# Kernel tuning notes

Measured on AMD Instinct MI355X. Metric: run time of the kernel, lower is better.

## Reference

```python
import jax, jax.numpy as jnp
import numpy as np

N_LAYERS = 2
D_MODEL = 1024
D_INNER = 2 * D_MODEL
D_STATE = 16
D_CONV = 4
DT_RANK = D_MODEL // 16  # 64
B_SZ, L = 1, 2048
EPS = 1e-5


def layernorm(x, w, b):
    mu = jnp.mean(x, axis=-1, keepdims=True)
    var = jnp.mean(jnp.square(x - mu), axis=-1, keepdims=True)
    return (x - mu) * jax.lax.rsqrt(var + EPS) * w + b


def mamba(x, in_w, cw, cb, xp_w, dtp_w, dtp_b, A_log, Dp, out_w):
    # x: [B, L, D_MODEL]
    Bn, Ln, _ = x.shape
    xz = jnp.einsum('bld,ed->ble', x, in_w)          # [B,L,2*D_INNER]
    xc, z = jnp.split(xz, 2, axis=-1)
    # causal depthwise conv1d (kernel D_CONV)
    xp = jnp.pad(xc, ((0, 0), (D_CONV - 1, 0), (0, 0)))
    xc = sum(xp[:, k:k + Ln, :] * cw[:, k] for k in range(D_CONV)) + cb
    xc = jax.nn.silu(xc)
    dbl = jnp.einsum('ble,re->blr', xc, xp_w)        # [B,L,DT_RANK+2*D_STATE]
    dt, Bm, Cm = jnp.split(dbl, [DT_RANK, DT_RANK + D_STATE], axis=-1)
    dt = jax.nn.softplus(jnp.einsum('blr,er->ble', dt, dtp_w) + dtp_b)  # [B,L,E]
    A = -jnp.exp(A_log)                              # [E,N], strictly negative
    dA = jnp.exp(dt[..., None] * A)                  # [B,L,E,N]
    dBu = (dt * xc)[..., None] * Bm[:, :, None, :]   # [B,L,E,N]

    def step(h, inp):
        dA_t, dBu_t, C_t = inp
        h = dA_t * h + dBu_t                         # [B,E,N]
        y = jnp.einsum('ben,bn->be', h, C_t)
        return h, y

    h0 = jnp.zeros((Bn, D_INNER, D_STATE), dA.dtype)
    _, ys = jax.lax.scan(step, h0, (dA.transpose(1, 0, 2, 3),
                                    dBu.transpose(1, 0, 2, 3),
                                    Cm.transpose(1, 0, 2)))
    y = ys.transpose(1, 0, 2) + xc * Dp              # [B,L,E]
    y = y * jax.nn.silu(z)
    return jnp.einsum('ble,de->bld', y, out_w)       # [B,L,D_MODEL]


def setup_inputs() -> dict:
    key = jax.random.key(0)
    ks = jax.random.split(key, 12)
    s = 0.02
    dt_init = np.log(np.expm1(0.01)).astype(np.float32)  # softplus^-1(0.01)
    A_row = jnp.log(jnp.arange(1, D_STATE + 1, dtype=jnp.float32))
    return {
        'x': jax.random.normal(ks[0], (B_SZ, L, D_MODEL), jnp.float32),
        'ln_w': jnp.ones((N_LAYERS, D_MODEL), jnp.float32),
        'ln_b': jnp.zeros((N_LAYERS, D_MODEL), jnp.float32),
        'in_proj_w': jax.random.normal(ks[1], (N_LAYERS, 2 * D_INNER, D_MODEL)) * s,
        'conv_w': jax.random.normal(ks[2], (N_LAYERS, D_INNER, D_CONV)) * 0.2,
        'conv_b': jnp.zeros((N_LAYERS, D_INNER), jnp.float32),
        'x_proj_w': jax.random.normal(ks[3], (N_LAYERS, DT_RANK + 2 * D_STATE, D_INNER)) * s,
        'dt_proj_w': jax.random.normal(ks[4], (N_LAYERS, D_INNER, DT_RANK)) * (DT_RANK ** -0.5),
        'dt_proj_b': jnp.full((N_LAYERS, D_INNER), dt_init),
        'A_log': jnp.broadcast_to(A_row, (N_LAYERS, D_INNER, D_STATE)).copy(),
        'D_skip': jnp.ones((N_LAYERS, D_INNER), jnp.float32),
        'out_proj_w': jax.random.normal(ks[5], (N_LAYERS, D_MODEL, D_INNER)) * s,
        'norm_f_w': jnp.ones((D_MODEL,), jnp.float32),
        'norm_f_b': jnp.zeros((D_MODEL,), jnp.float32),
    }


def reference(x, ln_w, ln_b, in_proj_w, conv_w, conv_b, x_proj_w, dt_proj_w,
              dt_proj_b, A_log, D_skip, out_proj_w, norm_f_w, norm_f_b):
    for i in range(N_LAYERS):
        h = layernorm(x, ln_w[i], ln_b[i])
        h = mamba(h, in_proj_w[i], conv_w[i], conv_b[i], x_proj_w[i],
                  dt_proj_w[i], dt_proj_b[i], A_log[i], D_skip[i], out_proj_w[i])
        x = h + x  # residual (dropout/drop_path are identity in eval)
    return layernorm(x, norm_f_w, norm_f_b)
```

## Files before the change

### kernel.cpp

```cpp
#include <hip/hip_runtime.h>
#include <hip/hip_bf16.h>
#include <math.h>

#define LSEQ 2048
#define DMODEL 1024
#define DINNER 2048
#define DSTATE 16
#define DCONV 4
#define DTRANK 64
#define RPROJ 96

#define CHUNK 32
#define NCHUNK (LSEQ / CHUNK)

#define XSPLIT 4

typedef __attribute__((ext_vector_type(8))) short bf16x8;
typedef __attribute__((ext_vector_type(4))) float f32x4;

__device__ __forceinline__ float softplusf(float x) {
    return (x > 20.f) ? x : log1pf(__expf(x));
}
__device__ __forceinline__ float siluf(float x) {
    return x / (1.f + __expf(-x));
}
__device__ __forceinline__ short f2bf(float f) {
    union { float f; unsigned u; } v; v.f = f;
    unsigned r = v.u + 0x7FFFu + ((v.u >> 16) & 1u);
    return (short)(r >> 16);
}
__device__ __forceinline__ float bf2f(short h) {
    union { unsigned u; float f; } v;
    v.u = ((unsigned)(unsigned short)h) << 16;
    return v.f;
}

__device__ __forceinline__ void cvt8(const float* __restrict__ s,
                                     short* __restrict__ d, int i) {
    const float4 a = *(const float4*)(s + i);
    const float4 b = *(const float4*)(s + i + 4);
    alignas(16) short h[8];
    h[0] = f2bf(a.x); h[1] = f2bf(a.y); h[2] = f2bf(a.z); h[3] = f2bf(a.w);
    h[4] = f2bf(b.x); h[5] = f2bf(b.y); h[6] = f2bf(b.z); h[7] = f2bf(b.w);
    *(uint4*)(d + i) = *(const uint4*)h;
}

__global__ __launch_bounds__(256) void cvt_weights(
    const float* __restrict__ s0, short* __restrict__ d0, int n0,
    const float* __restrict__ s1, short* __restrict__ d1, int n1,
    const float* __restrict__ s2, short* __restrict__ d2, int n2,
    const float* __restrict__ s3, short* __restrict__ d3, int n3)
{
    int i = (blockIdx.x * 256 + threadIdx.x) * 8;
    if (i < n0) { cvt8(s0, d0, i); return; }
    i -= n0;
    if (i < n1) { cvt8(s1, d1, i); return; }
    i -= n1;
    if (i < n2) { cvt8(s2, d2, i); return; }
    i -= n2;
    if (i < n3) { cvt8(s3, d3, i); return; }
}

__global__ __launch_bounds__(256) void ln_kernel(
    const float* __restrict__ x, const float* __restrict__ w,
    const float* __restrict__ b, float* __restrict__ outf,
    short* __restrict__ outb)
{
    __shared__ float s1[256], s2[256];
    const int row = blockIdx.x;
    const int tid = threadIdx.x;
    const float* xr = x + (size_t)row * DMODEL;
    float v[4];
    float s = 0.f, sq = 0.f;
#pragma unroll
    for (int k = 0; k < 4; k++) {
        v[k] = xr[k * 256 + tid];
        s += v[k];
        sq += v[k] * v[k];
    }
    s1[tid] = s; s2[tid] = sq;
    __syncthreads();
    for (int off = 128; off > 0; off >>= 1) {
        if (tid < off) { s1[tid] += s1[tid + off]; s2[tid] += s2[tid + off]; }
        __syncthreads();
    }
    const float mu = s1[0] * (1.f / DMODEL);
    const float var = s2[0] * (1.f / DMODEL) - mu * mu;
    const float rstd = rsqrtf(var + 1e-5f);
#pragma unroll
    for (int k = 0; k < 4; k++) {
        const int i = k * 256 + tid;
        const float o = (v[k] - mu) * rstd * w[i] + b[i];
        if (outf) outf[(size_t)row * DMODEL + i] = o;
        if (outb) outb[(size_t)row * DMODEL + i] = f2bf(o);
    }
}

template<int MODE>
__global__ __launch_bounds__(256) void gemm_mfma(
    const short* __restrict__ A, int lda,
    const short* __restrict__ W, int ldw,
    float* __restrict__ Cf, short* __restrict__ Cb, int ldc,
    int M, int N, int K,
    const float* __restrict__ bias,
    const float* __restrict__ resid,
    size_t csplit)
{
    __shared__ alignas(16) short As[64 * 32];
    __shared__ alignas(16) short Ws[64 * 32];

    const int tid = threadIdx.x;
    const int lane = tid & 63;
    const int w = tid >> 6;
    const int wr = w >> 1, wc = w & 1;
    const int row0 = blockIdx.y * 64;
    const int col0 = blockIdx.x * 64;
    const int kbeg = blockIdx.z * K;

    const int srow = tid >> 2;
    const int skch = ((tid & 3) ^ ((srow >> 1) & 3)) * 8;

    f32x4 acc[2][2];
#pragma unroll
    for (int i = 0; i < 2; i++)
#pragma unroll
        for (int j = 0; j < 2; j++) acc[i][j] = (f32x4)0.f;

    const int lrow = lane & 15;
    const int q = lane >> 4;
    const int wrow = col0 + srow;

    for (int kt = kbeg; kt < kbeg + K; kt += 32) {
        __syncthreads();
        {
            const short* gp = A + (size_t)(row0 + srow) * lda + kt + skch;
            __builtin_amdgcn_global_load_lds(
                (const __attribute__((address_space(1))) void*)gp,
                (__attribute__((address_space(3))) void*)(As + tid * 8), 16, 0, 0);
        }
        if (wrow < N) {
            const short* gp = W + (size_t)wrow * ldw + kt + skch;
            __builtin_amdgcn_global_load_lds(
                (const __attribute__((address_space(1))) void*)gp,
                (__attribute__((address_space(3))) void*)(Ws + tid * 8), 16, 0, 0);
        }
        __syncthreads();

        bf16x8 af[2], bfr[2];
#pragma unroll
        for (int i = 0; i < 2; i++) {
            const int R = wr * 32 + i * 16 + lrow;
            af[i] = *(const bf16x8*)&As[R * 32 + ((q ^ ((R >> 1) & 3)) * 8)];
        }
#pragma unroll
        for (int j = 0; j < 2; j++) {
            const int R = wc * 32 + j * 16 + lrow;
            bfr[j] = *(const bf16x8*)&Ws[R * 32 + ((q ^ ((R >> 1) & 3)) * 8)];
        }
#pragma unroll
        for (int i = 0; i < 2; i++)
#pragma unroll
            for (int j = 0; j < 2; j++)
                acc[i][j] = __builtin_amdgcn_mfma_f32_16x16x32_bf16(
                    af[i], bfr[j], acc[i][j], 0, 0, 0);
    }

    if (MODE == 0 && csplit) Cf += blockIdx.z * csplit;

    const int rbase = row0 + wr * 32;
    const int cbase = col0 + wc * 32;
#pragma unroll
    for (int i = 0; i < 2; i++) {
#pragma unroll
        for (int j = 0; j < 2; j++) {
            const int gcol = cbase + j * 16 + lrow;
            if (gcol < N) {
#pragma unroll
                for (int r = 0; r < 4; r++) {
                    const int grow = rbase + i * 16 + (lane >> 4) * 4 + r;
                    float v = acc[i][j][r];
                    if (MODE == 1) v = softplusf(v + bias[gcol]);
                    if (MODE == 2) v += resid[(size_t)grow * ldc + gcol];
                    if (MODE == 3) {
                        Cb[(size_t)grow * ldc + gcol] = f2bf(v);
                    } else {
                        Cf[(size_t)grow * ldc + gcol] = v;
                    }
                }
            }
        }
    }
}

__global__ __launch_bounds__(256) void combine_xproj(
    const float* __restrict__ part,
    float* __restrict__ dbl, short* __restrict__ dblb)
{
    const int i = (blockIdx.x * 256 + threadIdx.x) * 4;
    const int S = LSEQ * RPROJ;
    float4 v = *(const float4*)(part + i);
#pragma unroll
    for (int s = 1; s < XSPLIT; s++) {
        const float4 p = *(const float4*)(part + s * S + i);
        v.x += p.x; v.y += p.y; v.z += p.z; v.w += p.w;
    }
    *(float4*)(dbl + i) = v;
    alignas(8) short h[4] = {f2bf(v.x), f2bf(v.y), f2bf(v.z), f2bf(v.w)};
    *(unsigned long long*)(dblb + i) = *(const unsigned long long*)h;
}

__global__ __launch_bounds__(256) void conv_silu_kernel(
    const short* __restrict__ xzb, const float* __restrict__ cw,
    const float* __restrict__ cb, short* __restrict__ xcb)
{
    const int g = blockIdx.x * 256 + threadIdx.x;
    const int t = g >> 8;
    const int c0 = (g & 255) * 8;
    float acc[8];
#pragma unroll
    for (int j = 0; j < 8; j++) acc[j] = cb[c0 + j];
#pragma unroll
    for (int k = 0; k < DCONV; k++) {
        const int tt = t - (DCONV - 1) + k;
        if (tt >= 0) {
            const bf16x8 v = *(const bf16x8*)(xzb + (size_t)tt * (2 * DINNER) + c0);
#pragma unroll
            for (int j = 0; j < 8; j++)
                acc[j] += bf2f(v[j]) * cw[(c0 + j) * DCONV + k];
        }
    }
    alignas(16) short h[8];
#pragma unroll
    for (int j = 0; j < 8; j++) h[j] = f2bf(siluf(acc[j]));
    *(uint4*)(xcb + (size_t)t * DINNER + c0) = *(const uint4*)h;
}

__global__ __launch_bounds__(256) void scan_pass1(
    const float* __restrict__ dt,
    const short* __restrict__ xcb,
    const float* __restrict__ dbl,
    const float* __restrict__ A_log,
    float* __restrict__ S,
    float* __restrict__ sumdt)
{
    const int e = blockIdx.x * 256 + threadIdx.x;
    const int c = blockIdx.y;
    float a[DSTATE];
#pragma unroll
    for (int n = 0; n < DSTATE; n++) a[n] = -__expf(A_log[(size_t)e * DSTATE + n]);
    float h[DSTATE];
#pragma unroll
    for (int n = 0; n < DSTATE; n++) h[n] = 0.f;
    float sd = 0.f;

    __shared__ float sBC[CHUNK][32];
    for (int i = threadIdx.x; i < CHUNK * 32; i += 256) {
        const int tl = i >> 5, j = i & 31;
        sBC[tl][j] = dbl[(size_t)(c * CHUNK + tl) * RPROJ + DTRANK + j];
    }
    __syncthreads();

    for (int tl = 0; tl < CHUNK; tl++) {
        const int t = c * CHUNK + tl;
        const float dtv = dt[(size_t)t * DINNER + e];
        const float du = dtv * bf2f(xcb[(size_t)t * DINNER + e]);
        sd += dtv;
#pragma unroll
        for (int n = 0; n < DSTATE; n++) {
            const float dA = __expf(dtv * a[n]);
            h[n] = dA * h[n] + du * sBC[tl][n];
        }
    }
    sumdt[(size_t)c * DINNER + e] = sd;
#pragma unroll
    for (int n = 0; n < DSTATE; n++)
        S[((size_t)c * DSTATE + n) * DINNER + e] = h[n];
}

__global__ __launch_bounds__(256) void scan_pass2(
    const float* __restrict__ A_log,
    const float* __restrict__ sumdt,
    float* __restrict__ S)
{
    const int idx = blockIdx.x * 256 + threadIdx.x;
    const int e = idx & (DINNER - 1);
    const int n = idx >> 11;
    const float a = -__expf(A_log[(size_t)e * DSTATE + n]);
    float H = 0.f;
    for (int c = 0; c < NCHUNK; c++) {
        const size_t off = ((size_t)c * DSTATE + n) * DINNER + e;
        const float tmp = S[off];
        S[off] = H;
        const float P = __expf(a * sumdt[(size_t)c * DINNER + e]);
        H = P * H + tmp;
    }
}

__global__ __launch_bounds__(256) void scan_pass3(
    const float* __restrict__ dt,
    const short* __restrict__ xcb,
    const float* __restrict__ dbl,
    const short* __restrict__ xzb,
    const float* __restrict__ A_log,
    const float* __restrict__ Dp,
    const float* __restrict__ S,
    short* __restrict__ yb)
{
    const int e = blockIdx.x * 256 + threadIdx.x;
    const int c = blockIdx.y;
    float a[DSTATE];
#pragma unroll
    for (int n = 0; n < DSTATE; n++) a[n] = -__expf(A_log[(size_t)e * DSTATE + n]);
    float h[DSTATE];
#pragma unroll
    for (int n = 0; n < DSTATE; n++)
        h[n] = S[((size_t)c * DSTATE + n) * DINNER + e];
    const float dskip = Dp[e];

    __shared__ float sBC[CHUNK][32];
    for (int i = threadIdx.x; i < CHUNK * 32; i += 256) {
        const int tl = i >> 5, j = i & 31;
        sBC[tl][j] = dbl[(size_t)(c * CHUNK + tl) * RPROJ + DTRANK + j];
    }
    __syncthreads();

    for (int tl = 0; tl < CHUNK; tl++) {
        const int t = c * CHUNK + tl;
        const float dtv = dt[(size_t)t * DINNER + e];
        const float xcv = bf2f(xcb[(size_t)t * DINNER + e]);
        const float du = dtv * xcv;
        float yv = 0.f;
#pragma unroll
        for (int n = 0; n < DSTATE; n++) {
            const float dA = __expf(dtv * a[n]);
            h[n] = dA * h[n] + du * sBC[tl][n];
            yv += h[n] * sBC[tl][16 + n];
        }
        const float zv = bf2f(xzb[(size_t)t * (2 * DINNER) + DINNER + e]);
        yv = (yv + xcv * dskip) * siluf(zv);
        yb[(size_t)t * DINNER + e] = f2bf(yv);
    }
}

extern "C" void kernel_launch(void* const* d_in, const int* in_sizes, int n_in,
                              void* d_out, int out_size, void* d_ws, size_t ws_size,
                              hipStream_t stream) {
    const float* x_in   = (const float*)d_in[0];
    const float* ln_w   = (const float*)d_in[1];
    const float* ln_b   = (const float*)d_in[2];
    const float* in_w   = (const float*)d_in[3];
    const float* conv_w = (const float*)d_in[4];
    const float* conv_b = (const float*)d_in[5];
    const float* xp_w   = (const float*)d_in[6];
    const float* dtp_w  = (const float*)d_in[7];
    const float* dtp_b  = (const float*)d_in[8];
    const float* A_log  = (const float*)d_in[9];
    const float* D_skip = (const float*)d_in[10];
    const float* out_w  = (const float*)d_in[11];
    const float* nf_w   = (const float*)d_in[12];
    const float* nf_b   = (const float*)d_in[13];
    float* out = (float*)d_out;

    float* w = (float*)d_ws;
    float* buf_x = w; w += (size_t)LSEQ * DMODEL;
    float* dbl   = w; w += (size_t)LSEQ * RPROJ;
    float* xpart = w; w += (size_t)XSPLIT * LSEQ * RPROJ;
    float* dtb   = w; w += (size_t)LSEQ * DINNER;
    float* Sbuf  = w; w += (size_t)NCHUNK * DSTATE * DINNER;
    float* sumdt = w; w += (size_t)NCHUNK * DINNER;
    short* h_bf    = (short*)w; w += (size_t)LSEQ * DMODEL / 2;
    short* xz_bf   = (short*)w; w += (size_t)LSEQ * 2 * DINNER / 2;
    short* xc_bf   = (short*)w; w += (size_t)LSEQ * DINNER / 2;
    short* y_bf    = (short*)w; w += (size_t)LSEQ * DINNER / 2;
    short* dbl_bf  = (short*)w; w += (size_t)LSEQ * RPROJ / 2 + 1;
    short* in_w_bf  = (short*)w; w += (size_t)2 * (2 * DINNER) * DMODEL / 2;
    short* xp_w_bf  = (short*)w; w += (size_t)2 * RPROJ * DINNER / 2;
    short* dtp_w_bf = (short*)w; w += (size_t)2 * DINNER * DTRANK / 2;
    short* out_w_bf = (short*)w; w += (size_t)2 * DMODEL * DINNER / 2;

    {
        const int n1 = 2 * (2 * DINNER) * DMODEL;
        const int n2 = 2 * RPROJ * DINNER;
        const int n3 = 2 * DMODEL * DINNER;
        const int n4 = 2 * DINNER * DTRANK;
        const int total = n1 + n2 + n3 + n4;
        cvt_weights<<<dim3(total / (256 * 8)), dim3(256), 0, stream>>>(
            in_w, in_w_bf, n1, xp_w, xp_w_bf, n2,
            out_w, out_w_bf, n3, dtp_w, dtp_w_bf, n4);
    }

    for (int layer = 0; layer < 2; layer++) {
        const float* resid_src = (layer == 0) ? x_in : buf_x;
        ln_kernel<<<dim3(LSEQ), dim3(256), 0, stream>>>(
            resid_src, ln_w + layer * DMODEL, ln_b + layer * DMODEL,
            nullptr, h_bf);
        gemm_mfma<3><<<dim3((2 * DINNER) / 64, LSEQ / 64), dim3(256), 0, stream>>>(
            h_bf, DMODEL, in_w_bf + (size_t)layer * 2 * DINNER * DMODEL, DMODEL,
            nullptr, xz_bf, 2 * DINNER, LSEQ, 2 * DINNER, DMODEL, nullptr, nullptr, 0);
        conv_silu_kernel<<<dim3((LSEQ * DINNER / 8) / 256), dim3(256), 0, stream>>>(
            xz_bf, conv_w + (size_t)layer * DINNER * DCONV, conv_b + layer * DINNER,
            xc_bf);
        gemm_mfma<0><<<dim3(2, LSEQ / 64, XSPLIT), dim3(256), 0, stream>>>(
            xc_bf, DINNER, xp_w_bf + (size_t)layer * RPROJ * DINNER, DINNER,
            xpart, nullptr, RPROJ, LSEQ, RPROJ, DINNER / XSPLIT, nullptr, nullptr,
            (size_t)LSEQ * RPROJ);
        combine_xproj<<<dim3((LSEQ * RPROJ / 4) / 256), dim3(256), 0, stream>>>(
            xpart, dbl, dbl_bf);
        gemm_mfma<1><<<dim3(DINNER / 64, LSEQ / 64), dim3(256), 0, stream>>>(
            dbl_bf, RPROJ, dtp_w_bf + (size_t)layer * DINNER * DTRANK, DTRANK,
            dtb, nullptr, DINNER, LSEQ, DINNER, DTRANK,
            dtp_b + layer * DINNER, nullptr, 0);
        const float* Al = A_log + (size_t)layer * DINNER * DSTATE;
        scan_pass1<<<dim3(DINNER / 256, NCHUNK), dim3(256), 0, stream>>>(
            dtb, xc_bf, dbl, Al, Sbuf, sumdt);
        scan_pass2<<<dim3((DINNER * DSTATE) / 256), dim3(256), 0, stream>>>(
            Al, sumdt, Sbuf);
        scan_pass3<<<dim3(DINNER / 256, NCHUNK), dim3(256), 0, stream>>>(
            dtb, xc_bf, dbl, xz_bf, Al, D_skip + layer * DINNER, Sbuf, y_bf);
        gemm_mfma<2><<<dim3(DMODEL / 64, LSEQ / 64), dim3(256), 0, stream>>>(
            y_bf, DINNER, out_w_bf + (size_t)layer * DMODEL * DINNER, DINNER,
            buf_x, nullptr, DMODEL, LSEQ, DMODEL, DINNER, nullptr, resid_src, 0);
    }
    ln_kernel<<<dim3(LSEQ), dim3(256), 0, stream>>>(buf_x, nf_w, nf_b, out, nullptr);
}
```

Baseline: 517.1 us.

## Widen GEMM N-tiles, store dt in bf16, halve scan chunk, prefetch scan inputs

The GEMM kernel is templated on the number of 16-wide column fragments so the in_proj and dt_proj GEMMs use 64x128 tiles. This gives more MFMA work per A-tile load and launches fewer blocks. The dt projection now writes softplus output as bf16 rather than fp32, which halves dt traffic in both scan passes. The scan chunk drops from 32 to 16 to double parallelism, and the per-step loads in the scan passes are software-prefetched one step ahead. The trade-offs are bf16 rounding of dt before the exp, which may hurt accuracy, and twice the chunk-carry work in pass2.

New measurement: 491.1 us. 5.0% less time.

```diff
diff --git a/kernel.cpp b/kernel.cpp
--- a/kernel.cpp
+++ b/kernel.cpp
@@ -10,7 +10,7 @@
 #define DTRANK 64
 #define RPROJ 96
 
-#define CHUNK 32
+#define CHUNK 16
 #define NCHUNK (LSEQ / CHUNK)
 
 #define XSPLIT 4
@@ -96,7 +96,7 @@
     }
 }
 
-template<int MODE>
+template<int NJ, int MODE>
 __global__ __launch_bounds__(256) void gemm_mfma(
     const short* __restrict__ A, int lda,
     const short* __restrict__ W, int ldw,
@@ -106,29 +106,31 @@
     const float* __restrict__ resid,
     size_t csplit)
 {
+    constexpr int BN = 32 * NJ;
+    constexpr int HN = 16 * NJ;
+    constexpr int WISS = BN / 64;
     __shared__ alignas(16) short As[64 * 32];
-    __shared__ alignas(16) short Ws[64 * 32];
+    __shared__ alignas(16) short Ws[BN * 32];
 
     const int tid = threadIdx.x;
     const int lane = tid & 63;
     const int w = tid >> 6;
     const int wr = w >> 1, wc = w & 1;
     const int row0 = blockIdx.y * 64;
-    const int col0 = blockIdx.x * 64;
+    const int col0 = blockIdx.x * BN;
     const int kbeg = blockIdx.z * K;
 
     const int srow = tid >> 2;
     const int skch = ((tid & 3) ^ ((srow >> 1) & 3)) * 8;
 
-    f32x4 acc[2][2];
+    f32x4 acc[2][NJ];
 #pragma unroll
     for (int i = 0; i < 2; i++)
 #pragma unroll
-        for (int j = 0; j < 2; j++) acc[i][j] = (f32x4)0.f;
+        for (int j = 0; j < NJ; j++) acc[i][j] = (f32x4)0.f;
 
     const int lrow = lane & 15;
     const int q = lane >> 4;
-    const int wrow = col0 + srow;
 
     for (int kt = kbeg; kt < kbeg + K; kt += 32) {
         __syncthreads();
@@ -138,29 +140,34 @@
                 (const __attribute__((address_space(1))) void*)gp,
                 (__attribute__((address_space(3))) void*)(As + tid * 8), 16, 0, 0);
         }
-        if (wrow < N) {
-            const short* gp = W + (size_t)wrow * ldw + kt + skch;
-            __builtin_amdgcn_global_load_lds(
-                (const __attribute__((address_space(1))) void*)gp,
-                (__attribute__((address_space(3))) void*)(Ws + tid * 8), 16, 0, 0);
+#pragma unroll
+        for (int j = 0; j < WISS; j++) {
+            const int wrow = col0 + j * 64 + srow;
+            if (wrow < N) {
+                const short* gp = W + (size_t)wrow * ldw + kt + skch;
+                __builtin_amdgcn_global_load_lds(
+                    (const __attribute__((address_space(1))) void*)gp,
+                    (__attribute__((address_space(3))) void*)(Ws + j * 2048 + tid * 8),
+                    16, 0, 0);
+            }
         }
         __syncthreads();
 
-        bf16x8 af[2], bfr[2];
+        bf16x8 af[2], bfr[NJ];
 #pragma unroll
         for (int i = 0; i < 2; i++) {
             const int R = wr * 32 + i * 16 + lrow;
             af[i] = *(const bf16x8*)&As[R * 32 + ((q ^ ((R >> 1) & 3)) * 8)];
         }
 #pragma unroll
-        for (int j = 0; j < 2; j++) {
-            const int R = wc * 32 + j * 16 + lrow;
+        for (int j = 0; j < NJ; j++) {
+            const int R = wc * HN + j * 16 + lrow;
             bfr[j] = *(const bf16x8*)&Ws[R * 32 + ((q ^ ((R >> 1) & 3)) * 8)];
         }
 #pragma unroll
         for (int i = 0; i < 2; i++)
 #pragma unroll
-            for (int j = 0; j < 2; j++)
+            for (int j = 0; j < NJ; j++)
                 acc[i][j] = __builtin_amdgcn_mfma_f32_16x16x32_bf16(
                     af[i], bfr[j], acc[i][j], 0, 0, 0);
     }
@@ -168,20 +175,20 @@
     if (MODE == 0 && csplit) Cf += blockIdx.z * csplit;
 
     const int rbase = row0 + wr * 32;
-    const int cbase = col0 + wc * 32;
+    const int cbase = col0 + wc * HN;
 #pragma unroll
     for (int i = 0; i < 2; i++) {
 #pragma unroll
-        for (int j = 0; j < 2; j++) {
+        for (int j = 0; j < NJ; j++) {
             const int gcol = cbase + j * 16 + lrow;
             if (gcol < N) {
 #pragma unroll
                 for (int r = 0; r < 4; r++) {
                     const int grow = rbase + i * 16 + (lane >> 4) * 4 + r;
                     float v = acc[i][j][r];
-                    if (MODE == 1) v = softplusf(v + bias[gcol]);
                     if (MODE == 2) v += resid[(size_t)grow * ldc + gcol];
-                    if (MODE == 3) {
+                    if (MODE == 5) v = softplusf(v + bias[gcol]);
+                    if (MODE == 3 || MODE == 5) {
                         Cb[(size_t)grow * ldc + gcol] = f2bf(v);
                     } else {
                         Cf[(size_t)grow * ldc + gcol] = v;
@@ -236,7 +243,7 @@
 }
 
 __global__ __launch_bounds__(256) void scan_pass1(
-    const float* __restrict__ dt,
+    const short* __restrict__ dtb,
     const short* __restrict__ xcb,
     const float* __restrict__ dbl,
     const float* __restrict__ A_log,
@@ -260,16 +267,24 @@
     }
     __syncthreads();
 
+    const size_t rb = (size_t)c * CHUNK * DINNER + e;
+    short dt_c = dtb[rb], xc_c = xcb[rb];
+#pragma unroll
     for (int tl = 0; tl < CHUNK; tl++) {
-        const int t = c * CHUNK + tl;
-        const float dtv = dt[(size_t)t * DINNER + e];
-        const float du = dtv * bf2f(xcb[(size_t)t * DINNER + e]);
+        short dt_n = 0, xc_n = 0;
+        if (tl + 1 < CHUNK) {
+            dt_n = dtb[rb + (size_t)(tl + 1) * DINNER];
+            xc_n = xcb[rb + (size_t)(tl + 1) * DINNER];
+        }
+        const float dtv = bf2f(dt_c);
+        const float du = dtv * bf2f(xc_c);
         sd += dtv;
 #pragma unroll
         for (int n = 0; n < DSTATE; n++) {
             const float dA = __expf(dtv * a[n]);
             h[n] = dA * h[n] + du * sBC[tl][n];
         }
+        dt_c = dt_n; xc_c = xc_n;
     }
     sumdt[(size_t)c * DINNER + e] = sd;
 #pragma unroll
@@ -297,7 +312,7 @@
 }
 
 __global__ __launch_bounds__(256) void scan_pass3(
-    const float* __restrict__ dt,
+    const short* __restrict__ dtb,
     const short* __restrict__ xcb,
     const float* __restrict__ dbl,
     const short* __restrict__ xzb,
@@ -324,10 +339,19 @@
     }
     __syncthreads();
 
+    const size_t rb = (size_t)c * CHUNK * DINNER + e;
+    const size_t zb = (size_t)c * CHUNK * (2 * DINNER) + DINNER + e;
+    short dt_c = dtb[rb], xc_c = xcb[rb], z_c = xzb[zb];
+#pragma unroll
     for (int tl = 0; tl < CHUNK; tl++) {
-        const int t = c * CHUNK + tl;
-        const float dtv = dt[(size_t)t * DINNER + e];
-        const float xcv = bf2f(xcb[(size_t)t * DINNER + e]);
+        short dt_n = 0, xc_n = 0, z_n = 0;
+        if (tl + 1 < CHUNK) {
+            dt_n = dtb[rb + (size_t)(tl + 1) * DINNER];
+            xc_n = xcb[rb + (size_t)(tl + 1) * DINNER];
+            z_n = xzb[zb + (size_t)(tl + 1) * (2 * DINNER)];
+        }
+        const float dtv = bf2f(dt_c);
+        const float xcv = bf2f(xc_c);
         const float du = dtv * xcv;
         float yv = 0.f;
 #pragma unroll
@@ -336,9 +360,9 @@
             h[n] = dA * h[n] + du * sBC[tl][n];
             yv += h[n] * sBC[tl][16 + n];
         }
-        const float zv = bf2f(xzb[(size_t)t * (2 * DINNER) + DINNER + e]);
-        yv = (yv + xcv * dskip) * siluf(zv);
-        yb[(size_t)t * DINNER + e] = f2bf(yv);
+        yv = (yv + xcv * dskip) * siluf(bf2f(z_c));
+        yb[rb + (size_t)tl * DINNER] = f2bf(yv);
+        dt_c = dt_n; xc_c = xc_n; z_c = z_n;
     }
 }
 
@@ -365,12 +389,12 @@
     float* buf_x = w; w += (size_t)LSEQ * DMODEL;
     float* dbl   = w; w += (size_t)LSEQ * RPROJ;
     float* xpart = w; w += (size_t)XSPLIT * LSEQ * RPROJ;
-    float* dtb   = w; w += (size_t)LSEQ * DINNER;
     float* Sbuf  = w; w += (size_t)NCHUNK * DSTATE * DINNER;
     float* sumdt = w; w += (size_t)NCHUNK * DINNER;
     short* h_bf    = (short*)w; w += (size_t)LSEQ * DMODEL / 2;
     short* xz_bf   = (short*)w; w += (size_t)LSEQ * 2 * DINNER / 2;
     short* xc_bf   = (short*)w; w += (size_t)LSEQ * DINNER / 2;
+    short* dt_bf   = (short*)w; w += (size_t)LSEQ * DINNER / 2;
     short* y_bf    = (short*)w; w += (size_t)LSEQ * DINNER / 2;
     short* dbl_bf  = (short*)w; w += (size_t)LSEQ * RPROJ / 2 + 1;
     short* in_w_bf  = (short*)w; w += (size_t)2 * (2 * DINNER) * DMODEL / 2;
@@ -394,30 +418,30 @@
         ln_kernel<<<dim3(LSEQ), dim3(256), 0, stream>>>(
             resid_src, ln_w + layer * DMODEL, ln_b + layer * DMODEL,
             nullptr, h_bf);
-        gemm_mfma<3><<<dim3((2 * DINNER) / 64, LSEQ / 64), dim3(256), 0, stream>>>(
+        gemm_mfma<4, 3><<<dim3((2 * DINNER) / 128, LSEQ / 64), dim3(256), 0, stream>>>(
             h_bf, DMODEL, in_w_bf + (size_t)layer * 2 * DINNER * DMODEL, DMODEL,
             nullptr, xz_bf, 2 * DINNER, LSEQ, 2 * DINNER, DMODEL, nullptr, nullptr, 0);
         conv_silu_kernel<<<dim3((LSEQ * DINNER / 8) / 256), dim3(256), 0, stream>>>(
             xz_bf, conv_w + (size_t)layer * DINNER * DCONV, conv_b + layer * DINNER,
             xc_bf);
-        gemm_mfma<0><<<dim3(2, LSEQ / 64, XSPLIT), dim3(256), 0, stream>>>(
+        gemm_mfma<2, 0><<<dim3(2, LSEQ / 64, XSPLIT), dim3(256), 0, stream>>>(
             xc_bf, DINNER, xp_w_bf + (size_t)layer * RPROJ * DINNER, DINNER,
             xpart, nullptr, RPROJ, LSEQ, RPROJ, DINNER / XSPLIT, nullptr, nullptr,
             (size_t)LSEQ * RPROJ);
         combine_xproj<<<dim3((LSEQ * RPROJ / 4) / 256), dim3(256), 0, stream>>>(
             xpart, dbl, dbl_bf);
-        gemm_mfma<1><<<dim3(DINNER / 64, LSEQ / 64), dim3(256), 0, stream>>>(
+        gemm_mfma<4, 5><<<dim3(DINNER / 128, LSEQ / 64), dim3(256), 0, stream>>>(
             dbl_bf, RPROJ, dtp_w_bf + (size_t)layer * DINNER * DTRANK, DTRANK,
-            dtb, nullptr, DINNER, LSEQ, DINNER, DTRANK,
+            nullptr, dt_bf, DINNER, LSEQ, DINNER, DTRANK,
             dtp_b + layer * DINNER, nullptr, 0);
         const float* Al = A_log + (size_t)layer * DINNER * DSTATE;
         scan_pass1<<<dim3(DINNER / 256, NCHUNK), dim3(256), 0, stream>>>(
-            dtb, xc_bf, dbl, Al, Sbuf, sumdt);
+            dt_bf, xc_bf, dbl, Al, Sbuf, sumdt);
         scan_pass2<<<dim3((DINNER * DSTATE) / 256), dim3(256), 0, stream>>>(
             Al, sumdt, Sbuf);
         scan_pass3<<<dim3(DINNER / 256, NCHUNK), dim3(256), 0, stream>>>(
-            dtb, xc_bf, dbl, xz_bf, Al, D_skip + layer * DINNER, Sbuf, y_bf);
-        gemm_mfma<2><<<dim3(DMODEL / 64, LSEQ / 64), dim3(256), 0, stream>>>(
+            dt_bf, xc_bf, dbl, xz_bf, Al, D_skip + layer * DINNER, Sbuf, y_bf);
+        gemm_mfma<2, 2><<<dim3(DMODEL / 64, LSEQ / 64), dim3(256), 0, stream>>>(
             y_bf, DINNER, out_w_bf + (size_t)layer * DMODEL * DINNER, DINNER,
             buf_x, nullptr, DMODEL, LSEQ, DMODEL, DINNER, nullptr, resid_src, 0);
     }
```
